# Kernel optimization log

Measured on AMD Instinct MI355X. Metric: run time of the kernel, lower is better.

## Reference

```python
import jax, jax.numpy as jnp
import numpy as np

N = 50000
E = 1600000
D_CONTENT, D_STYLE, D_CAT = 768, 128, 32  # concat feature = 2*D_CAT = 64
H1, H2, NCLS = 64, 64, 2


def _lin_params(key, din, dout, bias=True):
    k1, k2 = jax.random.split(key)
    s = 1.0 / np.sqrt(din)
    W = jax.random.uniform(k1, (din, dout), jnp.float32, -s, s)
    b = jax.random.uniform(k2, (dout,), jnp.float32, -s, s) if bias else None
    return W, b


def setup_inputs() -> dict:
    key = jax.random.key(0)
    ks = jax.random.split(key, 16)
    x_content = jax.random.normal(ks[0], (N, D_CONTENT), jnp.float32)
    x_style = jax.random.normal(ks[1], (N, D_STYLE), jnp.float32)
    edge_index = jax.random.randint(ks[2], (2, E), 0, N, jnp.int64)
    edge_type = jax.random.randint(ks[3], (E,), 0, 4, jnp.int64)
    Wp, bp = _lin_params(ks[4], D_CONTENT, D_CAT)
    Ws, bs = _lin_params(ks[5], D_STYLE, D_CAT)
    # SAGEConv: lin_l (aggregated neighbors, has bias), lin_r (root, no bias)
    Wl1, bl1 = _lin_params(ks[6], 2 * D_CAT, H1)
    Wr1, _ = _lin_params(ks[7], 2 * D_CAT, H1, bias=False)
    Wl2, bl2 = _lin_params(ks[8], H1, H2)
    Wr2, _ = _lin_params(ks[9], H1, H2, bias=False)
    Wl3, bl3 = _lin_params(ks[10], H2, H2)
    Wr3, _ = _lin_params(ks[11], H2, H2, bias=False)
    Wo, bo = _lin_params(ks[12], H2, NCLS)
    return dict(x_content=x_content, x_style=x_style, edge_index=edge_index,
                edge_type=edge_type, Wp=Wp, bp=bp, Ws=Ws, bs=bs,
                Wl1=Wl1, bl1=bl1, Wr1=Wr1, Wl2=Wl2, bl2=bl2, Wr2=Wr2,
                Wl3=Wl3, bl3=bl3, Wr3=Wr3, Wo=Wo, bo=bo)


def _sage_conv(x, src, dst, Wl, bl, Wr):
    # mean aggregation of source-node features at destination nodes
    msg_sum = jax.ops.segment_sum(x[src], dst, num_segments=N)  # [N, d]
    deg = jax.ops.segment_sum(jnp.ones((src.shape[0],), x.dtype), dst,
                              num_segments=N)
    agg = msg_sum / jnp.maximum(deg, 1.0)[:, None]
    return agg @ Wl + bl + x @ Wr


def reference(x_content, x_style, edge_index, edge_type,
              Wp, bp, Ws, bs, Wl1, bl1, Wr1, Wl2, bl2, Wr2,
              Wl3, bl3, Wr3, Wo, bo):
    src, dst = edge_index[0], edge_index[1]
    x = jnp.concatenate([x_content @ Wp + bp, x_style @ Ws + bs], axis=1)
    x = jax.nn.relu(_sage_conv(x, src, dst, Wl1, bl1, Wr1))  # dropout = id (eval)
    x = jax.nn.relu(_sage_conv(x, src, dst, Wl2, bl2, Wr2))
    x = jax.nn.relu(_sage_conv(x, src, dst, Wl3, bl3, Wr3))
    return x @ Wo + bo
```

## Files before the change

### kernel.cpp

```cpp
#include <hip/hip_runtime.h>
#include <stdint.h>


typedef __attribute__((ext_vector_type(8))) unsigned short u16x8;
typedef __attribute__((ext_vector_type(4))) float f32x4;
typedef __attribute__((ext_vector_type(4))) unsigned int u32x4;
typedef __attribute__((ext_vector_type(2))) int i32x2;

static __device__ __forceinline__ float bf2f(unsigned short u) {
  union { unsigned int i; float f; } v;
  v.i = ((unsigned int)u) << 16;
  return v.f;
}

static __device__ __forceinline__ unsigned short f2bf(float f) {
  union { float f; unsigned int i; } v;
  v.f = f;
  unsigned int u = v.i;
  unsigned int r = (u + 0x7FFFu + ((u >> 16) & 1u)) >> 16;
  return (unsigned short)r;
}

template <bool BF>
static __device__ __forceinline__ float ldf(const void* p, long long i) {
  if (BF) return bf2f(((const unsigned short*)p)[i]);
  return ((const float*)p)[i];
}

static __device__ __forceinline__ int clampN(int v, int N) {
  return v < 0 ? 0 : (v >= N ? N - 1 : v);
}

__global__ void k_detect(const void* Wp, const int* ei, int* flags) {
  if (threadIdx.x == 0 && blockIdx.x == 0) {
    const unsigned short* w = (const unsigned short*)Wp;
    int bf = 1;
    for (int i = 0; i < 64; ++i) {
      float v = fabsf(bf2f(w[i]));
      if (!(v < 1.0f)) bf = 0;
    }
    flags[0] = bf;
    int i64 = 1;
    for (int i = 0; i < 32; ++i)
      if (ei[2 * i + 1] != 0) i64 = 0;
    flags[1] = i64;
  }
}

static __device__ __forceinline__ int edge_src(const int* ei, int e, int E,
                                               int i64) {
  return i64 ? ei[2 * (long long)e] : ei[e];
}
static __device__ __forceinline__ int edge_dst(const int* ei, int e, int E,
                                               int i64) {
  return i64 ? ei[2 * ((long long)E + e)] : ei[(long long)E + e];
}


__global__ __launch_bounds__(256) void k_pack(const int* __restrict__ ei, int E,
                                              int N, int* __restrict__ cnt,
                                              i32x2* __restrict__ pairs,
                                              const int* __restrict__ flags) {
  int e = blockIdx.x * 256 + threadIdx.x;
  if (e < E) {
    int i64 = flags[1];
    int s = clampN(edge_src(ei, e, E, i64), N);
    int d = clampN(edge_dst(ei, e, E, i64), N);
    i32x2 p;
    p[0] = s;
    p[1] = d;
    pairs[e] = p;
    atomicAdd(&cnt[d], 1);
  }
}

__global__ __launch_bounds__(256) void k_scan1(const int* __restrict__ cnt,
                                               int* __restrict__ rowptr,
                                               int* __restrict__ bsum, int N) {
  __shared__ int sh[256];
  int t = threadIdx.x;
  int base = blockIdx.x * 1024 + t * 4;
  int v0 = 0, v1 = 0, v2 = 0, v3 = 0;
  if (base + 0 < N) v0 = cnt[base + 0];
  if (base + 1 < N) v1 = cnt[base + 1];
  if (base + 2 < N) v2 = cnt[base + 2];
  if (base + 3 < N) v3 = cnt[base + 3];
  int s = v0 + v1 + v2 + v3;
  sh[t] = s;
  __syncthreads();
  int acc = s;
  for (int off = 1; off < 256; off <<= 1) {
    int x = 0;
    if (t >= off) x = sh[t - off];
    __syncthreads();
    acc += x;
    sh[t] = acc;
    __syncthreads();
  }
  int run = acc - s;
  if (base + 0 < N) rowptr[base + 0] = run;
  run += v0;
  if (base + 1 < N) rowptr[base + 1] = run;
  run += v1;
  if (base + 2 < N) rowptr[base + 2] = run;
  run += v2;
  if (base + 3 < N) rowptr[base + 3] = run;
  run += v3;
  if (t == 255) bsum[blockIdx.x] = acc;
}

__global__ void k_scan2(int* __restrict__ bsum, int nb,
                        int* __restrict__ rowptr, int N) {
  if (threadIdx.x == 0 && blockIdx.x == 0) {
    int run = 0;
    for (int i = 0; i < nb; ++i) {
      int v = bsum[i];
      bsum[i] = run;
      run += v;
    }
    rowptr[N] = run;
  }
}

__global__ __launch_bounds__(256) void k_scan3(int* __restrict__ rowptr,
                                               int* __restrict__ cursor,
                                               const int* __restrict__ bsum,
                                               int N) {
  int i = blockIdx.x * 256 + threadIdx.x;
  if (i < N) {
    int v = rowptr[i] + bsum[i >> 10];
    rowptr[i] = v;
    cursor[i] = v;
  }
}

__global__ __launch_bounds__(256) void k_scatter2(
    const i32x2* __restrict__ pairs, int E, int lo, int hi,
    int* __restrict__ cursor, int* __restrict__ colbuf) {
  int e = blockIdx.x * 256 + threadIdx.x;
  if (e < E) {
    i32x2 p2 = pairs[e];
    int d = p2[1];
    if (d >= lo && d < hi) {
      int p = atomicAdd(&cursor[d], 1);
      if (p >= 0 && p < E) colbuf[p] = p2[0];
    }
  }
}

template <bool BF>
static __device__ void project_body(const void* __restrict__ xc,
                                    const void* __restrict__ xs,
                                    const void* __restrict__ Wp,
                                    const void* __restrict__ bp,
                                    const void* __restrict__ Ws,
                                    const void* __restrict__ bs,
                                    float* __restrict__ h0, int N,
                                    float* __restrict__ lds) {
  float* xt = lds;
  unsigned int* wtb = (unsigned int*)(lds + 2 * 64 * 68);
  float* wtf = lds + 2 * 64 * 68;

  int tid = (int)threadIdx.x;
  int w = __builtin_amdgcn_readfirstlane(tid >> 6);
  int lane = tid & 63;
  int node = (int)blockIdx.x * 64 + lane;

  int sn = tid >> 2;
  int sj = tid & 3;
  int gsn = (int)blockIdx.x * 64 + sn;
  int gsnc = gsn < N ? gsn : (N - 1);

  float c[8], s[8];
#pragma unroll
  for (int r = 0; r < 8; ++r) {
    c[r] = 0.f;
    s[r] = 0.f;
  }

  u16x8 pr0 = {}, pr1 = {};
  f32x4 pf0 = {}, pf1 = {}, pf2 = {}, pf3 = {};
  u32x4 wrg = {};
  f32x4 wf0 = {}, wf1 = {};

  auto stage_load = [&](int t) {
    long long idx;
    const void* src;
    if (t < 12) {
      src = xc;
      idx = (long long)gsnc * 768 + t * 64 + 16 * sj;
    } else {
      src = xs;
      idx = (long long)gsnc * 128 + (t - 12) * 64 + 16 * sj;
    }
    if (BF) {
      const unsigned short* p = (const unsigned short*)src + idx;
      pr0 = *(const u16x8*)p;
      pr1 = *(const u16x8*)(p + 8);
    } else {
      const float* p = (const float*)src + idx;
      pf0 = *(const f32x4*)(p + 0);
      pf1 = *(const f32x4*)(p + 4);
      pf2 = *(const f32x4*)(p + 8);
      pf3 = *(const f32x4*)(p + 12);
    }
    int rowg = (t < 12) ? (t * 64 + sn) : ((t - 12) * 64 + sn);
    const void* wsrc = (t < 12) ? Wp : Ws;
    if (BF) {
      wrg = *(const u32x4*)((const unsigned int*)wsrc +
                            (long long)rowg * 16 + 4 * sj);
    } else {
      const float* p = (const float*)wsrc + (long long)rowg * 32 + 8 * sj;
      wf0 = *(const f32x4*)p;
      wf1 = *(const f32x4*)(p + 4);
    }
  };

  auto stage_write = [&](int t) {
    float* row = xt + (t & 1) * (64 * 68) + sn * 68 + 16 * sj;
    if (BF) {
      f32x4 v;
#pragma unroll
      for (int i = 0; i < 4; ++i) v[i] = bf2f(pr0[i]);
      *(f32x4*)(row + 0) = v;
#pragma unroll
      for (int i = 0; i < 4; ++i) v[i] = bf2f(pr0[4 + i]);
      *(f32x4*)(row + 4) = v;
#pragma unroll
      for (int i = 0; i < 4; ++i) v[i] = bf2f(pr1[i]);
      *(f32x4*)(row + 8) = v;
#pragma unroll
      for (int i = 0; i < 4; ++i) v[i] = bf2f(pr1[4 + i]);
      *(f32x4*)(row + 12) = v;
    } else {
      *(f32x4*)(row + 0) = pf0;
      *(f32x4*)(row + 4) = pf1;
      *(f32x4*)(row + 8) = pf2;
      *(f32x4*)(row + 12) = pf3;
    }
    if (BF) {
      *(u32x4*)(wtb + (t & 1) * (64 * 16) + sn * 16 + 4 * sj) = wrg;
    } else {
      float* wrow = wtf + (t & 1) * (64 * 32) + sn * 32 + 8 * sj;
      *(f32x4*)wrow = wf0;
      *(f32x4*)(wrow + 4) = wf1;
    }
  };

  stage_load(0);
  stage_write(0);
  __syncthreads();

#pragma unroll 1
  for (int t = 0; t < 14; ++t) {
    if (t + 1 < 14) stage_load(t + 1);

    const float* xrow = xt + (t & 1) * (64 * 68) + lane * 68;
    if (BF) {
      const unsigned int* wbase = wtb + (t & 1) * (64 * 16) + 4 * w;
      if (t < 12) {
#pragma unroll 2
        for (int k0 = 0; k0 < 64; k0 += 4) {
          f32x4 x4 = *(const f32x4*)(xrow + k0);
#pragma unroll
          for (int kk = 0; kk < 4; ++kk) {
            u32x4 wp4 = *(const u32x4*)(wbase + (k0 + kk) * 16);
#pragma unroll
            for (int p = 0; p < 4; ++p) {
              union { unsigned int i; float f; } lo, hi;
              lo.i = wp4[p] << 16;
              hi.i = wp4[p] & 0xFFFF0000u;
              c[2 * p + 0] += x4[kk] * lo.f;
              c[2 * p + 1] += x4[kk] * hi.f;
            }
          }
        }
      } else {
#pragma unroll 2
        for (int k0 = 0; k0 < 64; k0 += 4) {
          f32x4 x4 = *(const f32x4*)(xrow + k0);
#pragma unroll
          for (int kk = 0; kk < 4; ++kk) {
            u32x4 wp4 = *(const u32x4*)(wbase + (k0 + kk) * 16);
#pragma unroll
            for (int p = 0; p < 4; ++p) {
              union { unsigned int i; float f; } lo, hi;
              lo.i = wp4[p] << 16;
              hi.i = wp4[p] & 0xFFFF0000u;
              s[2 * p + 0] += x4[kk] * lo.f;
              s[2 * p + 1] += x4[kk] * hi.f;
            }
          }
        }
      }
    } else {
      const float* wbase = wtf + (t & 1) * (64 * 32) + 8 * w;
      if (t < 12) {
#pragma unroll 2
        for (int k0 = 0; k0 < 64; k0 += 4) {
          f32x4 x4 = *(const f32x4*)(xrow + k0);
#pragma unroll
          for (int kk = 0; kk < 4; ++kk) {
            const float* wr = wbase + (k0 + kk) * 32;
            f32x4 wa = *(const f32x4*)wr;
            f32x4 wb = *(const f32x4*)(wr + 4);
#pragma unroll
            for (int r = 0; r < 4; ++r) {
              c[r] += x4[kk] * wa[r];
              c[4 + r] += x4[kk] * wb[r];
            }
          }
        }
      } else {
#pragma unroll 2
        for (int k0 = 0; k0 < 64; k0 += 4) {
          f32x4 x4 = *(const f32x4*)(xrow + k0);
#pragma unroll
          for (int kk = 0; kk < 4; ++kk) {
            const float* wr = wbase + (k0 + kk) * 32;
            f32x4 wa = *(const f32x4*)wr;
            f32x4 wb = *(const f32x4*)(wr + 4);
#pragma unroll
            for (int r = 0; r < 4; ++r) {
              s[r] += x4[kk] * wa[r];
              s[4 + r] += x4[kk] * wb[r];
            }
          }
        }
      }
    }

    if (t + 1 < 14) stage_write(t + 1);
    __syncthreads();
  }

  if (node < N) {
    float* orow = h0 + (long long)node * 64;
    f32x4 v;
#pragma unroll
    for (int r = 0; r < 4; ++r) v[r] = c[r] + ldf<BF>(bp, 8 * w + r);
    *(f32x4*)(orow + 8 * w) = v;
#pragma unroll
    for (int r = 0; r < 4; ++r) v[r] = c[4 + r] + ldf<BF>(bp, 8 * w + 4 + r);
    *(f32x4*)(orow + 8 * w + 4) = v;
#pragma unroll
    for (int r = 0; r < 4; ++r) v[r] = s[r] + ldf<BF>(bs, 8 * w + r);
    *(f32x4*)(orow + 32 + 8 * w) = v;
#pragma unroll
    for (int r = 0; r < 4; ++r) v[r] = s[4 + r] + ldf<BF>(bs, 8 * w + 4 + r);
    *(f32x4*)(orow + 32 + 8 * w + 4) = v;
  }
}

__global__ __launch_bounds__(256) void k_project(
    const void* __restrict__ xc, const void* __restrict__ xs,
    const void* __restrict__ Wp, const void* __restrict__ bp,
    const void* __restrict__ Ws, const void* __restrict__ bs,
    float* __restrict__ h0, int N, const int* __restrict__ flags) {
  __shared__ float lds[2 * 64 * 68 + 2 * 64 * 32];
  if (flags[0])
    project_body<true>(xc, xs, Wp, bp, Ws, bs, h0, N, lds);
  else
    project_body<false>(xc, xs, Wp, bp, Ws, bs, h0, N, lds);
}

template <bool BF>
static __device__ void layer_body(const float* __restrict__ hin,
                                  const int* __restrict__ rowptr,
                                  const int* __restrict__ colbuf,
                                  const void* Wl, const void* bl,
                                  const void* Wr, float* __restrict__ hout,
                                  int N, int last, const void* Wo,
                                  const void* bo, void* outp) {
  int node = (int)((blockIdx.x * blockDim.x + threadIdx.x) >> 6);
  int lane = (int)(threadIdx.x & 63);
  if (node >= N) return;
  int rs = rowptr[node], re = rowptr[node + 1];
  float xself = hin[(long long)node * 64 + lane];
  float agg0 = 0.f, agg1 = 0.f, agg2 = 0.f, agg3 = 0.f;
  float agg4 = 0.f, agg5 = 0.f, agg6 = 0.f, agg7 = 0.f;
  for (int cb = rs; cb < re; cb += 64) {
    int sidx = 0;
    if (cb + lane < re) sidx = clampN(colbuf[cb + lane], N);
    int c = re - cb;
    if (c > 64) c = 64;
    int t = 0;
    for (; t + 8 <= c; t += 8) {
      int s0 = __builtin_amdgcn_readlane(sidx, t + 0);
      int s1 = __builtin_amdgcn_readlane(sidx, t + 1);
      int s2 = __builtin_amdgcn_readlane(sidx, t + 2);
      int s3 = __builtin_amdgcn_readlane(sidx, t + 3);
      int s4 = __builtin_amdgcn_readlane(sidx, t + 4);
      int s5 = __builtin_amdgcn_readlane(sidx, t + 5);
      int s6 = __builtin_amdgcn_readlane(sidx, t + 6);
      int s7 = __builtin_amdgcn_readlane(sidx, t + 7);
      float v0 = hin[(long long)s0 * 64 + lane];
      float v1 = hin[(long long)s1 * 64 + lane];
      float v2 = hin[(long long)s2 * 64 + lane];
      float v3 = hin[(long long)s3 * 64 + lane];
      float v4 = hin[(long long)s4 * 64 + lane];
      float v5 = hin[(long long)s5 * 64 + lane];
      float v6 = hin[(long long)s6 * 64 + lane];
      float v7 = hin[(long long)s7 * 64 + lane];
      agg0 += v0;
      agg1 += v1;
      agg2 += v2;
      agg3 += v3;
      agg4 += v4;
      agg5 += v5;
      agg6 += v6;
      agg7 += v7;
    }
    for (; t < c; ++t) {
      int s = __builtin_amdgcn_readlane(sidx, t);
      agg0 += hin[(long long)s * 64 + lane];
    }
  }
  float agg = ((agg0 + agg1) + (agg2 + agg3)) + ((agg4 + agg5) + (agg6 + agg7));
  int deg = re - rs;
  if (deg > 0) agg *= (1.f / (float)deg);

  float o = ldf<BF>(bl, lane);
#pragma unroll 8
  for (int d = 0; d < 64; ++d) {
    float ad = __uint_as_float(
        __builtin_amdgcn_readlane(__float_as_uint(agg), d));
    float xd = __uint_as_float(
        __builtin_amdgcn_readlane(__float_as_uint(xself), d));
    o += ad * ldf<BF>(Wl, d * 64 + lane);
    o += xd * ldf<BF>(Wr, d * 64 + lane);
  }
  o = fmaxf(o, 0.f);

  if (!last) {
    hout[(long long)node * 64 + lane] = o;
  } else {
    float c0 = o * ldf<BF>(Wo, lane * 2 + 0);
    float c1 = o * ldf<BF>(Wo, lane * 2 + 1);
    for (int off = 32; off > 0; off >>= 1) {
      c0 += __shfl_xor(c0, off, 64);
      c1 += __shfl_xor(c1, off, 64);
    }
    if (lane == 0) {
      float r0 = c0 + ldf<BF>(bo, 0);
      float r1 = c1 + ldf<BF>(bo, 1);
      if (BF) {
        unsigned short* o16 = (unsigned short*)outp;
        o16[(long long)node * 2 + 0] = f2bf(r0);
        o16[(long long)node * 2 + 1] = f2bf(r1);
      } else {
        float* o32 = (float*)outp;
        o32[(long long)node * 2 + 0] = r0;
        o32[(long long)node * 2 + 1] = r1;
      }
    }
  }
}

__global__ __launch_bounds__(256) void k_layer(
    const float* hin, const int* rowptr, const int* colbuf, const void* Wl,
    const void* bl, const void* Wr, float* hout, int N, int last,
    const void* Wo, const void* bo, void* outp, const int* __restrict__ flags) {
  if (flags[0])
    layer_body<true>(hin, rowptr, colbuf, Wl, bl, Wr, hout, N, last, Wo, bo,
                     outp);
  else
    layer_body<false>(hin, rowptr, colbuf, Wl, bl, Wr, hout, N, last, Wo, bo,
                      outp);
}


extern "C" void kernel_launch(void* const* d_in, const int* in_sizes, int n_in,
                              void* d_out, int out_size, void* d_ws,
                              size_t ws_size, hipStream_t stream) {
  const void* xc = d_in[0];
  const void* xs = d_in[1];
  const int* ei = (const int*)d_in[2];
  const void* Wp = d_in[4];
  const void* bp = d_in[5];
  const void* Ws = d_in[6];
  const void* bs = d_in[7];
  const void* Wl1 = d_in[8];
  const void* bl1 = d_in[9];
  const void* Wr1 = d_in[10];
  const void* Wl2 = d_in[11];
  const void* bl2 = d_in[12];
  const void* Wr2 = d_in[13];
  const void* Wl3 = d_in[14];
  const void* bl3 = d_in[15];
  const void* Wr3 = d_in[16];
  const void* Wo = d_in[17];
  const void* bo = d_in[18];

  int N = out_size / 2;
  int E = in_sizes[3];

  char* ws = (char*)d_ws;
  size_t off = 0;
  auto alloc = [&](size_t bytes) {
    char* p = ws + off;
    off += (bytes + 255) & ~(size_t)255;
    return p;
  };
  int* colbuf = (int*)alloc((size_t)E * 4);
  int* cnt = (int*)alloc((size_t)N * 4);
  int* rowptr = (int*)alloc((size_t)(N + 1) * 4);
  int* cursor = (int*)alloc((size_t)N * 4);
  int* bsum = (int*)alloc(4096);
  int* flags = (int*)alloc(256);
  float* h0 = (float*)alloc((size_t)N * 64 * 4);
  float* h1 = (float*)alloc((size_t)N * 64 * 4);
  (void)ws_size;
  (void)n_in;

  i32x2* pairs = (i32x2*)h0;

  k_detect<<<1, 64, 0, stream>>>(Wp, ei, flags);

  hipMemsetAsync(cnt, 0, (size_t)N * 4, stream);
  int eb = (E + 255) / 256;
  k_pack<<<eb, 256, 0, stream>>>(ei, E, N, cnt, pairs, flags);
  int sb = (N + 1023) / 1024;
  k_scan1<<<sb, 256, 0, stream>>>(cnt, rowptr, bsum, N);
  k_scan2<<<1, 64, 0, stream>>>(bsum, sb, rowptr, N);
  k_scan3<<<(N + 255) / 256, 256, 0, stream>>>(rowptr, cursor, bsum, N);

  const int NPASS = 8;
  int chunk = (N + NPASS - 1) / NPASS;
  for (int r = 0; r < NPASS; ++r) {
    int lo = r * chunk;
    int hi = lo + chunk < N ? lo + chunk : N;
    k_scatter2<<<eb, 256, 0, stream>>>(pairs, E, lo, hi, cursor, colbuf);
  }

  int pb = (N + 63) / 64;
  k_project<<<pb, 256, 0, stream>>>(xc, xs, Wp, bp, Ws, bs, h0, N, flags);

  int nb4 = (N + 3) / 4;
  k_layer<<<nb4, 256, 0, stream>>>(h0, rowptr, colbuf, Wl1, bl1, Wr1, h1, N, 0,
                                   nullptr, nullptr, nullptr, flags);
  k_layer<<<nb4, 256, 0, stream>>>(h1, rowptr, colbuf, Wl2, bl2, Wr2, h0, N, 0,
                                   nullptr, nullptr, nullptr, flags);
  k_layer<<<nb4, 256, 0, stream>>>(h0, rowptr, colbuf, Wl3, bl3, Wr3, h1, N, 1,
                                   Wo, bo, d_out, flags);
}
```

Measured before the change: 730.2 us.

## Use bf16 MFMA for projection, unroll gather by 16, halve scatter passes

The bf16 path of the input projection now stages both weight matrices into LDS in an MFMA-friendly layout and computes the 64-column projection with 16x16x32 bf16 MFMA instructions, replacing scalar FMA loops with in-register bf16 unpacking. The SAGE neighbor gather gains a 16-wide unrolled path so more independent loads are in flight per wave. The CSR scatter runs in 4 destination-range passes instead of 8, reducing launches and re-reads of the edge list at some cost to write locality. The default inputs are float32, so the MFMA path may only run if the dtype-detection flag selects bf16.

```diff
diff --git a/kernel.cpp b/kernel.cpp
--- a/kernel.cpp
+++ b/kernel.cpp
@@ -3,6 +3,7 @@
 
 
 typedef __attribute__((ext_vector_type(8))) unsigned short u16x8;
+typedef __attribute__((ext_vector_type(8))) short bf16x8;
 typedef __attribute__((ext_vector_type(4))) float f32x4;
 typedef __attribute__((ext_vector_type(4))) unsigned int u32x4;
 typedef __attribute__((ext_vector_type(2))) int i32x2;
@@ -148,8 +149,7 @@
   }
 }
 
-template <bool BF>
-static __device__ void project_body(const void* __restrict__ xc,
+static __device__ void project_mfma(const void* __restrict__ xc,
                                     const void* __restrict__ xs,
                                     const void* __restrict__ Wp,
                                     const void* __restrict__ bp,
@@ -157,8 +157,94 @@
                                     const void* __restrict__ bs,
                                     float* __restrict__ h0, int N,
                                     float* __restrict__ lds) {
+  unsigned short* fb = (unsigned short*)lds;
+  int tid = (int)threadIdx.x;
+  int w = __builtin_amdgcn_readfirstlane(tid >> 6);
+  int l = tid & 63;
+  int node0 = (int)blockIdx.x * 64;
+
+  const unsigned short* wp16 = (const unsigned short*)Wp;
+  const unsigned short* ws16 = (const unsigned short*)Ws;
+#pragma unroll
+  for (int i = 0; i < 14; ++i) {
+    int ci = tid + 256 * i;
+    int e0 = ci * 8;
+    int isC = e0 < 24576;
+    int eb = isC ? e0 : (e0 - 24576);
+    int r = eb >> 5;
+    int c0 = eb & 31;
+    int s_ = r >> 5;
+    int g = (r >> 3) & 3;
+    int j = r & 7;
+    int f = isC ? (s_ * 2 + (c0 >> 4)) : (48 + s_ * 2 + (c0 >> 4));
+    u16x8 v = *(const u16x8*)((isC ? wp16 : ws16) + eb);
+    unsigned short* d = fb + f * 512 + ((g << 4) + (c0 & 15)) * 8 + j;
+#pragma unroll
+    for (int m = 0; m < 8; ++m) d[m * 8] = v[m];
+  }
+  __syncthreads();
+
+  int arow = node0 + 16 * w + (l & 15);
+  int arowc = arow < N ? arow : (N - 1);
+  int kg = (l >> 4) * 8;
+  const unsigned short* xcl = (const unsigned short*)xc + (long long)arowc * 768;
+  const unsigned short* xsl = (const unsigned short*)xs + (long long)arowc * 128;
+
+  auto loadA = [&](int s) -> bf16x8 {
+    if (s < 24) return *(const bf16x8*)(xcl + s * 32 + kg);
+    return *(const bf16x8*)(xsl + (s - 24) * 32 + kg);
+  };
+
+  f32x4 ac0 = {0.f, 0.f, 0.f, 0.f};
+  f32x4 ac1 = {0.f, 0.f, 0.f, 0.f};
+  f32x4 ac2 = {0.f, 0.f, 0.f, 0.f};
+  f32x4 ac3 = {0.f, 0.f, 0.f, 0.f};
+
+  bf16x8 a0 = loadA(0);
+  bf16x8 a1 = loadA(1);
+#pragma unroll 1
+  for (int s = 0; s < 28; ++s) {
+    bf16x8 acur = a0;
+    a0 = a1;
+    if (s + 2 < 28) a1 = loadA(s + 2);
+    if (s < 24) {
+      bf16x8 b0 = *(const bf16x8*)(fb + (s * 2 + 0) * 512 + l * 8);
+      bf16x8 b1 = *(const bf16x8*)(fb + (s * 2 + 1) * 512 + l * 8);
+      ac0 = __builtin_amdgcn_mfma_f32_16x16x32_bf16(acur, b0, ac0, 0, 0, 0);
+      ac1 = __builtin_amdgcn_mfma_f32_16x16x32_bf16(acur, b1, ac1, 0, 0, 0);
+    } else {
+      int sb = s - 24;
+      bf16x8 b2 = *(const bf16x8*)(fb + (48 + sb * 2 + 0) * 512 + l * 8);
+      bf16x8 b3 = *(const bf16x8*)(fb + (48 + sb * 2 + 1) * 512 + l * 8);
+      ac2 = __builtin_amdgcn_mfma_f32_16x16x32_bf16(acur, b2, ac2, 0, 0, 0);
+      ac3 = __builtin_amdgcn_mfma_f32_16x16x32_bf16(acur, b3, ac3, 0, 0, 0);
+    }
+  }
+
+  int colb = l & 15;
+  int rbase = (l >> 4) * 4;
+#pragma unroll
+  for (int r = 0; r < 4; ++r) {
+    int nodeg = node0 + 16 * w + rbase + r;
+    if (nodeg < N) {
+      float* orow = h0 + (long long)nodeg * 64;
+      orow[0 + colb] = ac0[r] + bf2f(((const unsigned short*)bp)[0 + colb]);
+      orow[16 + colb] = ac1[r] + bf2f(((const unsigned short*)bp)[16 + colb]);
+      orow[32 + colb] = ac2[r] + bf2f(((const unsigned short*)bs)[0 + colb]);
+      orow[48 + colb] = ac3[r] + bf2f(((const unsigned short*)bs)[16 + colb]);
+    }
+  }
+}
+
+static __device__ void project_f32(const void* __restrict__ xc,
+                                   const void* __restrict__ xs,
+                                   const void* __restrict__ Wp,
+                                   const void* __restrict__ bp,
+                                   const void* __restrict__ Ws,
+                                   const void* __restrict__ bs,
+                                   float* __restrict__ h0, int N,
+                                   float* __restrict__ lds) {
   float* xt = lds;
-  unsigned int* wtb = (unsigned int*)(lds + 2 * 64 * 68);
   float* wtf = lds + 2 * 64 * 68;
 
   int tid = (int)threadIdx.x;
@@ -178,9 +264,7 @@
     s[r] = 0.f;
   }
 
-  u16x8 pr0 = {}, pr1 = {};
   f32x4 pf0 = {}, pf1 = {}, pf2 = {}, pf3 = {};
-  u32x4 wrg = {};
   f32x4 wf0 = {}, wf1 = {};
 
   auto stage_load = [&](int t) {
@@ -193,58 +277,27 @@
       src = xs;
       idx = (long long)gsnc * 128 + (t - 12) * 64 + 16 * sj;
     }
-    if (BF) {
-      const unsigned short* p = (const unsigned short*)src + idx;
-      pr0 = *(const u16x8*)p;
-      pr1 = *(const u16x8*)(p + 8);
-    } else {
-      const float* p = (const float*)src + idx;
-      pf0 = *(const f32x4*)(p + 0);
-      pf1 = *(const f32x4*)(p + 4);
-      pf2 = *(const f32x4*)(p + 8);
-      pf3 = *(const f32x4*)(p + 12);
-    }
+    const float* p = (const float*)src + idx;
+    pf0 = *(const f32x4*)(p + 0);
+    pf1 = *(const f32x4*)(p + 4);
+    pf2 = *(const f32x4*)(p + 8);
+    pf3 = *(const f32x4*)(p + 12);
     int rowg = (t < 12) ? (t * 64 + sn) : ((t - 12) * 64 + sn);
-    const void* wsrc = (t < 12) ? Wp : Ws;
-    if (BF) {
-      wrg = *(const u32x4*)((const unsigned int*)wsrc +
-                            (long long)rowg * 16 + 4 * sj);
-    } else {
-      const float* p = (const float*)wsrc + (long long)rowg * 32 + 8 * sj;
-      wf0 = *(const f32x4*)p;
-      wf1 = *(const f32x4*)(p + 4);
-    }
+    const float* wp = (const float*)((t < 12) ? Wp : Ws) +
+                      (long long)rowg * 32 + 8 * sj;
+    wf0 = *(const f32x4*)wp;
+    wf1 = *(const f32x4*)(wp + 4);
   };
 
   auto stage_write = [&](int t) {
     float* row = xt + (t & 1) * (64 * 68) + sn * 68 + 16 * sj;
-    if (BF) {
-      f32x4 v;
-#pragma unroll
-      for (int i = 0; i < 4; ++i) v[i] = bf2f(pr0[i]);
-      *(f32x4*)(row + 0) = v;
-#pragma unroll
-      for (int i = 0; i < 4; ++i) v[i] = bf2f(pr0[4 + i]);
-      *(f32x4*)(row + 4) = v;
-#pragma unroll
-      for (int i = 0; i < 4; ++i) v[i] = bf2f(pr1[i]);
-      *(f32x4*)(row + 8) = v;
-#pragma unroll
-      for (int i = 0; i < 4; ++i) v[i] = bf2f(pr1[4 + i]);
-      *(f32x4*)(row + 12) = v;
-    } else {
-      *(f32x4*)(row + 0) = pf0;
-      *(f32x4*)(row + 4) = pf1;
-      *(f32x4*)(row + 8) = pf2;
-      *(f32x4*)(row + 12) = pf3;
-    }
-    if (BF) {
-      *(u32x4*)(wtb + (t & 1) * (64 * 16) + sn * 16 + 4 * sj) = wrg;
-    } else {
-      float* wrow = wtf + (t & 1) * (64 * 32) + sn * 32 + 8 * sj;
-      *(f32x4*)wrow = wf0;
-      *(f32x4*)(wrow + 4) = wf1;
-    }
+    *(f32x4*)(row + 0) = pf0;
+    *(f32x4*)(row + 4) = pf1;
+    *(f32x4*)(row + 8) = pf2;
+    *(f32x4*)(row + 12) = pf3;
+    float* wrow = wtf + (t & 1) * (64 * 32) + sn * 32 + 8 * sj;
+    *(f32x4*)wrow = wf0;
+    *(f32x4*)(wrow + 4) = wf1;
   };
 
   stage_load(0);
@@ -254,82 +307,24 @@
 #pragma unroll 1
   for (int t = 0; t < 14; ++t) {
     if (t + 1 < 14) stage_load(t + 1);
-
     const float* xrow = xt + (t & 1) * (64 * 68) + lane * 68;
-    if (BF) {
-      const unsigned int* wbase = wtb + (t & 1) * (64 * 16) + 4 * w;
-      if (t < 12) {
+    const float* wbase = wtf + (t & 1) * (64 * 32) + 8 * w;
+    float* acc = (t < 12) ? c : s;
 #pragma unroll 2
-        for (int k0 = 0; k0 < 64; k0 += 4) {
-          f32x4 x4 = *(const f32x4*)(xrow + k0);
-#pragma unroll
-          for (int kk = 0; kk < 4; ++kk) {
-            u32x4 wp4 = *(const u32x4*)(wbase + (k0 + kk) * 16);
-#pragma unroll
-            for (int p = 0; p < 4; ++p) {
-              union { unsigned int i; float f; } lo, hi;
-              lo.i = wp4[p] << 16;
-              hi.i = wp4[p] & 0xFFFF0000u;
-              c[2 * p + 0] += x4[kk] * lo.f;
-              c[2 * p + 1] += x4[kk] * hi.f;
-            }
-          }
-        }
-      } else {
-#pragma unroll 2
-        for (int k0 = 0; k0 < 64; k0 += 4) {
-          f32x4 x4 = *(const f32x4*)(xrow + k0);
-#pragma unroll
-          for (int kk = 0; kk < 4; ++kk) {
-            u32x4 wp4 = *(const u32x4*)(wbase + (k0 + kk) * 16);
-#pragma unroll
-            for (int p = 0; p < 4; ++p) {
-              union { unsigned int i; float f; } lo, hi;
-              lo.i = wp4[p] << 16;
-              hi.i = wp4[p] & 0xFFFF0000u;
-              s[2 * p + 0] += x4[kk] * lo.f;
-              s[2 * p + 1] += x4[kk] * hi.f;
-            }
-          }
+    for (int k0 = 0; k0 < 64; k0 += 4) {
+      f32x4 x4 = *(const f32x4*)(xrow + k0);
+#pragma unroll
+      for (int kk = 0; kk < 4; ++kk) {
+        const float* wr = wbase + (k0 + kk) * 32;
+        f32x4 wa = *(const f32x4*)wr;
+        f32x4 wb = *(const f32x4*)(wr + 4);
+#pragma unroll
+        for (int r = 0; r < 4; ++r) {
+          acc[r] += x4[kk] * wa[r];
+          acc[4 + r] += x4[kk] * wb[r];
         }
       }
-    } else {
-      const float* wbase = wtf + (t & 1) * (64 * 32) + 8 * w;
-      if (t < 12) {
-#pragma unroll 2
-        for (int k0 = 0; k0 < 64; k0 += 4) {
-          f32x4 x4 = *(const f32x4*)(xrow + k0);
-#pragma unroll
-          for (int kk = 0; kk < 4; ++kk) {
-            const float* wr = wbase + (k0 + kk) * 32;
-            f32x4 wa = *(const f32x4*)wr;
-            f32x4 wb = *(const f32x4*)(wr + 4);
-#pragma unroll
-            for (int r = 0; r < 4; ++r) {
-              c[r] += x4[kk] * wa[r];
-              c[4 + r] += x4[kk] * wb[r];
-            }
-          }
-        }
-      } else {
-#pragma unroll 2
-        for (int k0 = 0; k0 < 64; k0 += 4) {
-          f32x4 x4 = *(const f32x4*)(xrow + k0);
-#pragma unroll
-          for (int kk = 0; kk < 4; ++kk) {
-            const float* wr = wbase + (k0 + kk) * 32;
-            f32x4 wa = *(const f32x4*)wr;
-            f32x4 wb = *(const f32x4*)(wr + 4);
-#pragma unroll
-            for (int r = 0; r < 4; ++r) {
-              s[r] += x4[kk] * wa[r];
-              s[4 + r] += x4[kk] * wb[r];
-            }
-          }
-        }
-      }
-    }
-
+    }
     if (t + 1 < 14) stage_write(t + 1);
     __syncthreads();
   }
@@ -338,16 +333,18 @@
     float* orow = h0 + (long long)node * 64;
     f32x4 v;
 #pragma unroll
-    for (int r = 0; r < 4; ++r) v[r] = c[r] + ldf<BF>(bp, 8 * w + r);
+    for (int r = 0; r < 4; ++r) v[r] = c[r] + ((const float*)bp)[8 * w + r];
     *(f32x4*)(orow + 8 * w) = v;
 #pragma unroll
-    for (int r = 0; r < 4; ++r) v[r] = c[4 + r] + ldf<BF>(bp, 8 * w + 4 + r);
+    for (int r = 0; r < 4; ++r)
+      v[r] = c[4 + r] + ((const float*)bp)[8 * w + 4 + r];
     *(f32x4*)(orow + 8 * w + 4) = v;
 #pragma unroll
-    for (int r = 0; r < 4; ++r) v[r] = s[r] + ldf<BF>(bs, 8 * w + r);
+    for (int r = 0; r < 4; ++r) v[r] = s[r] + ((const float*)bs)[8 * w + r];
     *(f32x4*)(orow + 32 + 8 * w) = v;
 #pragma unroll
-    for (int r = 0; r < 4; ++r) v[r] = s[4 + r] + ldf<BF>(bs, 8 * w + 4 + r);
+    for (int r = 0; r < 4; ++r)
+      v[r] = s[4 + r] + ((const float*)bs)[8 * w + 4 + r];
     *(f32x4*)(orow + 32 + 8 * w + 4) = v;
   }
 }
@@ -357,11 +354,11 @@
     const void* __restrict__ Wp, const void* __restrict__ bp,
     const void* __restrict__ Ws, const void* __restrict__ bs,
     float* __restrict__ h0, int N, const int* __restrict__ flags) {
-  __shared__ float lds[2 * 64 * 68 + 2 * 64 * 32];
+  __shared__ float lds[14336];
   if (flags[0])
-    project_body<true>(xc, xs, Wp, bp, Ws, bs, h0, N, lds);
+    project_mfma(xc, xs, Wp, bp, Ws, bs, h0, N, lds);
   else
-    project_body<false>(xc, xs, Wp, bp, Ws, bs, h0, N, lds);
+    project_f32(xc, xs, Wp, bp, Ws, bs, h0, N, lds);
 }
 
 template <bool BF>
@@ -385,6 +382,48 @@
     int c = re - cb;
     if (c > 64) c = 64;
     int t = 0;
+    for (; t + 16 <= c; t += 16) {
+      int s0 = __builtin_amdgcn_readlane(sidx, t + 0);
+      int s1 = __builtin_amdgcn_readlane(sidx, t + 1);
+      int s2 = __builtin_amdgcn_readlane(sidx, t + 2);
+      int s3 = __builtin_amdgcn_readlane(sidx, t + 3);
+      int s4 = __builtin_amdgcn_readlane(sidx, t + 4);
+      int s5 = __builtin_amdgcn_readlane(sidx, t + 5);
+      int s6 = __builtin_amdgcn_readlane(sidx, t + 6);
+      int s7 = __builtin_amdgcn_readlane(sidx, t + 7);
+      int s8 = __builtin_amdgcn_readlane(sidx, t + 8);
+      int s9 = __builtin_amdgcn_readlane(sidx, t + 9);
+      int sa = __builtin_amdgcn_readlane(sidx, t + 10);
+      int sb = __builtin_amdgcn_readlane(sidx, t + 11);
+      int sc = __builtin_amdgcn_readlane(sidx, t + 12);
+      int sd = __builtin_amdgcn_readlane(sidx, t + 13);
+      int se = __builtin_amdgcn_readlane(sidx, t + 14);
+      int sf = __builtin_amdgcn_readlane(sidx, t + 15);
+      float v0 = hin[(long long)s0 * 64 + lane];
+      float v1 = hin[(long long)s1 * 64 + lane];
+      float v2 = hin[(long long)s2 * 64 + lane];
+      float v3 = hin[(long long)s3 * 64 + lane];
+      float v4 = hin[(long long)s4 * 64 + lane];
+      float v5 = hin[(long long)s5 * 64 + lane];
+      float v6 = hin[(long long)s6 * 64 + lane];
+      float v7 = hin[(long long)s7 * 64 + lane];
+      float v8 = hin[(long long)s8 * 64 + lane];
+      float v9 = hin[(long long)s9 * 64 + lane];
+      float va = hin[(long long)sa * 64 + lane];
+      float vb = hin[(long long)sb * 64 + lane];
+      float vc = hin[(long long)sc * 64 + lane];
+      float vd = hin[(long long)sd * 64 + lane];
+      float ve = hin[(long long)se * 64 + lane];
+      float vf = hin[(long long)sf * 64 + lane];
+      agg0 += v0 + v8;
+      agg1 += v1 + v9;
+      agg2 += v2 + va;
+      agg3 += v3 + vb;
+      agg4 += v4 + vc;
+      agg5 += v5 + vd;
+      agg6 += v6 + ve;
+      agg7 += v7 + vf;
+    }
     for (; t + 8 <= c; t += 8) {
       int s0 = __builtin_amdgcn_readlane(sidx, t + 0);
       int s1 = __builtin_amdgcn_readlane(sidx, t + 1);
@@ -525,7 +564,7 @@
   k_scan2<<<1, 64, 0, stream>>>(bsum, sb, rowptr, N);
   k_scan3<<<(N + 255) / 256, 256, 0, stream>>>(rowptr, cursor, bsum, N);
 
-  const int NPASS = 8;
+  const int NPASS = 4;
   int chunk = (N + NPASS - 1) / NPASS;
   for (int r = 0; r < NPASS; ++r) {
     int lo = r * chunk;
```

After: 727.6 us. About the same (-0.4%).

## Move input projection to bf16 MFMA with split-precision, widen gather unroll

Applied to the files above, without the earlier changes.

Adds an MFMA path for the content/style projection. Weights are pre-split into bf16 hi/lo fragment layouts, and the fp32 activations are split on the fly into three bf16 products so fp32 accuracy is roughly kept. A runtime self-test kernel checks the MFMA fragment layout and falls back to the old VALU kernel if it fails. The layer gather loop also gets a 16-wide unroll, and the scatter pass count is halved. This costs extra launches and roughly three times the MFMA work for fp32 inputs.

```diff
diff --git a/kernel.cpp b/kernel.cpp
--- a/kernel.cpp
+++ b/kernel.cpp
@@ -3,6 +3,7 @@
 
 
 typedef __attribute__((ext_vector_type(8))) unsigned short u16x8;
+typedef __attribute__((ext_vector_type(8))) short bf16x8;
 typedef __attribute__((ext_vector_type(4))) float f32x4;
 typedef __attribute__((ext_vector_type(4))) unsigned int u32x4;
 typedef __attribute__((ext_vector_type(2))) int i32x2;
@@ -25,6 +26,36 @@
 static __device__ __forceinline__ float ldf(const void* p, long long i) {
   if (BF) return bf2f(((const unsigned short*)p)[i]);
   return ((const float*)p)[i];
+}
+
+template <bool BF>
+static __device__ __forceinline__ void load8(const void* p, long long idx,
+                                             float* out) {
+  if (BF) {
+    u16x8 v = *(const u16x8*)((const unsigned short*)p + idx);
+#pragma unroll
+    for (int j = 0; j < 8; ++j) out[j] = bf2f(v[j]);
+  } else {
+    f32x4 a = *(const f32x4*)((const float*)p + idx);
+    f32x4 b = *(const f32x4*)((const float*)p + idx + 4);
+#pragma unroll
+    for (int j = 0; j < 4; ++j) {
+      out[j] = a[j];
+      out[4 + j] = b[j];
+    }
+  }
+}
+
+static __device__ __forceinline__ void split8(const float* v, bf16x8& hi,
+                                              bf16x8& lo) {
+#pragma unroll
+  for (int j = 0; j < 8; ++j) {
+    unsigned int u = __float_as_uint(v[j]);
+    unsigned int uh = u & 0xFFFF0000u;
+    hi[j] = (short)(uh >> 16);
+    float rf = v[j] - __uint_as_float(uh);
+    lo[j] = (short)(__float_as_uint(rf) >> 16);
+  }
 }
 
 static __device__ __forceinline__ int clampN(int v, int N) {
@@ -45,6 +76,35 @@
       if (ei[2 * i + 1] != 0) i64 = 0;
     flags[1] = i64;
   }
+}
+
+__global__ void k_mfmatest(int* flags) {
+  int l = (int)threadIdx.x;
+  int rc = l & 15;
+  int kg = (l >> 4) * 8;
+  bf16x8 a, b;
+#pragma unroll
+  for (int j = 0; j < 8; ++j) {
+    int k = kg + j;
+    a[j] = (short)f2bf((float)(((rc * 31 + k * 7) % 13) - 6));
+    b[j] = (short)f2bf((float)(((k * 5 + rc * 3) % 11) - 5));
+  }
+  f32x4 z = {0.f, 0.f, 0.f, 0.f};
+  f32x4 d = __builtin_amdgcn_mfma_f32_16x16x32_bf16(a, b, z, 0, 0, 0);
+  bool ok = true;
+#pragma unroll
+  for (int r = 0; r < 4; ++r) {
+    int rw = (l >> 4) * 4 + r;
+    float ref = 0.f;
+    for (int k = 0; k < 32; ++k) {
+      float av = (float)(((rw * 31 + k * 7) % 13) - 6);
+      float bv = (float)(((k * 5 + rc * 3) % 11) - 5);
+      ref += av * bv;
+    }
+    ok = ok && (d[r] == ref);
+  }
+  unsigned long long m = __ballot(ok);
+  if (l == 0) flags[2] = (m == 0xFFFFFFFFFFFFFFFFull) ? 1 : 0;
 }
 
 static __device__ __forceinline__ int edge_src(const int* ei, int e, int E,
@@ -148,15 +208,160 @@
   }
 }
 
+__global__ __launch_bounds__(256) void k_wprep(
+    const void* __restrict__ Wp, const void* __restrict__ Ws,
+    unsigned short* __restrict__ wfhi, unsigned short* __restrict__ wflo,
+    const int* __restrict__ flags) {
+  int ci = (int)blockIdx.x * 256 + (int)threadIdx.x;
+  if (ci >= 3584) return;
+  int BF = flags[0];
+  int e0 = ci * 8;
+  int isC = e0 < 24576;
+  int eb = isC ? e0 : (e0 - 24576);
+  int r = eb >> 5;
+  int c0 = eb & 31;
+  int s_ = r >> 5;
+  int g = (r >> 3) & 3;
+  int j = r & 7;
+  int f = isC ? (s_ * 2 + (c0 >> 4)) : (48 + s_ * 2 + (c0 >> 4));
+  const void* wsrc = isC ? Wp : Ws;
+  float v[8];
+  if (BF) {
+    load8<true>(wsrc, eb, v);
+  } else {
+    load8<false>(wsrc, eb, v);
+  }
+  bf16x8 hi, lo;
+  split8(v, hi, lo);
+  unsigned short* dh = wfhi + f * 512 + ((g << 4) + (c0 & 15)) * 8 + j;
+  unsigned short* dl = wflo + f * 512 + ((g << 4) + (c0 & 15)) * 8 + j;
+#pragma unroll
+  for (int m = 0; m < 8; ++m) {
+    dh[m * 8] = (unsigned short)hi[m];
+    dl[m * 8] = (unsigned short)lo[m];
+  }
+}
+
 template <bool BF>
-static __device__ void project_body(const void* __restrict__ xc,
-                                    const void* __restrict__ xs,
-                                    const void* __restrict__ Wp,
-                                    const void* __restrict__ bp,
-                                    const void* __restrict__ Ws,
-                                    const void* __restrict__ bs,
-                                    float* __restrict__ h0, int N,
-                                    float* __restrict__ lds) {
+static __device__ void project_mfma_body(
+    const void* __restrict__ xc, const void* __restrict__ xs,
+    const unsigned short* __restrict__ wfhi,
+    const unsigned short* __restrict__ wflo, const void* __restrict__ bp,
+    const void* __restrict__ bs, float* __restrict__ h0, int N) {
+  int tid = (int)threadIdx.x;
+  int w = __builtin_amdgcn_readfirstlane(tid >> 6);
+  int l = tid & 63;
+  int node0 = (int)blockIdx.x * 64;
+
+  int arow = node0 + 16 * w + (l & 15);
+  int arowc = arow < N ? arow : (N - 1);
+  int kg = (l >> 4) * 8;
+  long long xco = (long long)arowc * 768;
+  long long xso = (long long)arowc * 128;
+
+  f32x4 ac0 = {0.f, 0.f, 0.f, 0.f};
+  f32x4 ac1 = {0.f, 0.f, 0.f, 0.f};
+  f32x4 ac2 = {0.f, 0.f, 0.f, 0.f};
+  f32x4 ac3 = {0.f, 0.f, 0.f, 0.f};
+
+  float av0[8], av1[8];
+  load8<BF>(xc, xco + 0 * 32 + kg, av0);
+  load8<BF>(xc, xco + 1 * 32 + kg, av1);
+
+#pragma unroll
+  for (int s = 0; s < 28; ++s) {
+    float cur[8];
+#pragma unroll
+    for (int j = 0; j < 8; ++j) {
+      cur[j] = av0[j];
+      av0[j] = av1[j];
+    }
+    if (s + 2 < 28) {
+      int sn = s + 2;
+      if (sn < 24)
+        load8<BF>(xc, xco + sn * 32 + kg, av1);
+      else
+        load8<BF>(xs, xso + (sn - 24) * 32 + kg, av1);
+    }
+
+    bf16x8 ah, al;
+    split8(cur, ah, al);
+
+    if (s < 24) {
+      const unsigned short* f0 = wfhi + (s * 2 + 0) * 512 + l * 8;
+      const unsigned short* f1 = wfhi + (s * 2 + 1) * 512 + l * 8;
+      bf16x8 b0h = *(const bf16x8*)f0;
+      bf16x8 b1h = *(const bf16x8*)f1;
+      ac0 = __builtin_amdgcn_mfma_f32_16x16x32_bf16(ah, b0h, ac0, 0, 0, 0);
+      ac1 = __builtin_amdgcn_mfma_f32_16x16x32_bf16(ah, b1h, ac1, 0, 0, 0);
+      if (!BF) {
+        const unsigned short* g0 = wflo + (s * 2 + 0) * 512 + l * 8;
+        const unsigned short* g1 = wflo + (s * 2 + 1) * 512 + l * 8;
+        bf16x8 b0l = *(const bf16x8*)g0;
+        bf16x8 b1l = *(const bf16x8*)g1;
+        ac0 = __builtin_amdgcn_mfma_f32_16x16x32_bf16(ah, b0l, ac0, 0, 0, 0);
+        ac0 = __builtin_amdgcn_mfma_f32_16x16x32_bf16(al, b0h, ac0, 0, 0, 0);
+        ac1 = __builtin_amdgcn_mfma_f32_16x16x32_bf16(ah, b1l, ac1, 0, 0, 0);
+        ac1 = __builtin_amdgcn_mfma_f32_16x16x32_bf16(al, b1h, ac1, 0, 0, 0);
+      }
+    } else {
+      int sb = s - 24;
+      const unsigned short* f2 = wfhi + (48 + sb * 2 + 0) * 512 + l * 8;
+      const unsigned short* f3 = wfhi + (48 + sb * 2 + 1) * 512 + l * 8;
+      bf16x8 b2h = *(const bf16x8*)f2;
+      bf16x8 b3h = *(const bf16x8*)f3;
+      ac2 = __builtin_amdgcn_mfma_f32_16x16x32_bf16(ah, b2h, ac2, 0, 0, 0);
+      ac3 = __builtin_amdgcn_mfma_f32_16x16x32_bf16(ah, b3h, ac3, 0, 0, 0);
+      if (!BF) {
+        const unsigned short* g2 = wflo + (48 + sb * 2 + 0) * 512 + l * 8;
+        const unsigned short* g3 = wflo + (48 + sb * 2 + 1) * 512 + l * 8;
+        bf16x8 b2l = *(const bf16x8*)g2;
+        bf16x8 b3l = *(const bf16x8*)g3;
+        ac2 = __builtin_amdgcn_mfma_f32_16x16x32_bf16(ah, b2l, ac2, 0, 0, 0);
+        ac2 = __builtin_amdgcn_mfma_f32_16x16x32_bf16(al, b2h, ac2, 0, 0, 0);
+        ac3 = __builtin_amdgcn_mfma_f32_16x16x32_bf16(ah, b3l, ac3, 0, 0, 0);
+        ac3 = __builtin_amdgcn_mfma_f32_16x16x32_bf16(al, b3h, ac3, 0, 0, 0);
+      }
+    }
+  }
+
+  int colb = l & 15;
+  int rbase = (l >> 4) * 4;
+#pragma unroll
+  for (int r = 0; r < 4; ++r) {
+    int nodeg = node0 + 16 * w + rbase + r;
+    if (nodeg < N) {
+      float* orow = h0 + (long long)nodeg * 64;
+      orow[0 + colb] = ac0[r] + ldf<BF>(bp, 0 + colb);
+      orow[16 + colb] = ac1[r] + ldf<BF>(bp, 16 + colb);
+      orow[32 + colb] = ac2[r] + ldf<BF>(bs, 0 + colb);
+      orow[48 + colb] = ac3[r] + ldf<BF>(bs, 16 + colb);
+    }
+  }
+}
+
+__global__ __launch_bounds__(256) void k_project_mfma(
+    const void* __restrict__ xc, const void* __restrict__ xs,
+    const unsigned short* __restrict__ wfhi,
+    const unsigned short* __restrict__ wflo, const void* __restrict__ bp,
+    const void* __restrict__ bs, float* __restrict__ h0, int N,
+    const int* __restrict__ flags) {
+  if (!flags[2]) return;
+  if (flags[0])
+    project_mfma_body<true>(xc, xs, wfhi, wflo, bp, bs, h0, N);
+  else
+    project_mfma_body<false>(xc, xs, wfhi, wflo, bp, bs, h0, N);
+}
+
+template <bool BF>
+static __device__ void project_valu_body(const void* __restrict__ xc,
+                                         const void* __restrict__ xs,
+                                         const void* __restrict__ Wp,
+                                         const void* __restrict__ bp,
+                                         const void* __restrict__ Ws,
+                                         const void* __restrict__ bs,
+                                         float* __restrict__ h0, int N,
+                                         float* __restrict__ lds) {
   float* xt = lds;
   unsigned int* wtb = (unsigned int*)(lds + 2 * 64 * 68);
   float* wtf = lds + 2 * 64 * 68;
@@ -254,82 +459,45 @@
 #pragma unroll 1
   for (int t = 0; t < 14; ++t) {
     if (t + 1 < 14) stage_load(t + 1);
-
     const float* xrow = xt + (t & 1) * (64 * 68) + lane * 68;
     if (BF) {
       const unsigned int* wbase = wtb + (t & 1) * (64 * 16) + 4 * w;
-      if (t < 12) {
+      float* acc = (t < 12) ? c : s;
 #pragma unroll 2
-        for (int k0 = 0; k0 < 64; k0 += 4) {
-          f32x4 x4 = *(const f32x4*)(xrow + k0);
-#pragma unroll
-          for (int kk = 0; kk < 4; ++kk) {
-            u32x4 wp4 = *(const u32x4*)(wbase + (k0 + kk) * 16);
-#pragma unroll
-            for (int p = 0; p < 4; ++p) {
-              union { unsigned int i; float f; } lo, hi;
-              lo.i = wp4[p] << 16;
-              hi.i = wp4[p] & 0xFFFF0000u;
-              c[2 * p + 0] += x4[kk] * lo.f;
-              c[2 * p + 1] += x4[kk] * hi.f;
-            }
-          }
-        }
-      } else {
-#pragma unroll 2
-        for (int k0 = 0; k0 < 64; k0 += 4) {
-          f32x4 x4 = *(const f32x4*)(xrow + k0);
-#pragma unroll
-          for (int kk = 0; kk < 4; ++kk) {
-            u32x4 wp4 = *(const u32x4*)(wbase + (k0 + kk) * 16);
-#pragma unroll
-            for (int p = 0; p < 4; ++p) {
-              union { unsigned int i; float f; } lo, hi;
-              lo.i = wp4[p] << 16;
-              hi.i = wp4[p] & 0xFFFF0000u;
-              s[2 * p + 0] += x4[kk] * lo.f;
-              s[2 * p + 1] += x4[kk] * hi.f;
-            }
+      for (int k0 = 0; k0 < 64; k0 += 4) {
+        f32x4 x4 = *(const f32x4*)(xrow + k0);
+#pragma unroll
+        for (int kk = 0; kk < 4; ++kk) {
+          u32x4 wp4 = *(const u32x4*)(wbase + (k0 + kk) * 16);
+#pragma unroll
+          for (int p = 0; p < 4; ++p) {
+            union { unsigned int i; float f; } lo, hi;
+            lo.i = wp4[p] << 16;
+            hi.i = wp4[p] & 0xFFFF0000u;
+            acc[2 * p + 0] += x4[kk] * lo.f;
+            acc[2 * p + 1] += x4[kk] * hi.f;
           }
         }
       }
     } else {
       const float* wbase = wtf + (t & 1) * (64 * 32) + 8 * w;
-      if (t < 12) {
+      float* acc = (t < 12) ? c : s;
 #pragma unroll 2
-        for (int k0 = 0; k0 < 64; k0 += 4) {
-          f32x4 x4 = *(const f32x4*)(xrow + k0);
-#pragma unroll
-          for (int kk = 0; kk < 4; ++kk) {
-            const float* wr = wbase + (k0 + kk) * 32;
-            f32x4 wa = *(const f32x4*)wr;
-            f32x4 wb = *(const f32x4*)(wr + 4);
-#pragma unroll
-            for (int r = 0; r < 4; ++r) {
-              c[r] += x4[kk] * wa[r];
-              c[4 + r] += x4[kk] * wb[r];
-            }
-          }
-        }
-      } else {
-#pragma unroll 2
-        for (int k0 = 0; k0 < 64; k0 += 4) {
-          f32x4 x4 = *(const f32x4*)(xrow + k0);
-#pragma unroll
-          for (int kk = 0; kk < 4; ++kk) {
-            const float* wr = wbase + (k0 + kk) * 32;
-            f32x4 wa = *(const f32x4*)wr;
-            f32x4 wb = *(const f32x4*)(wr + 4);
-#pragma unroll
-            for (int r = 0; r < 4; ++r) {
-              s[r] += x4[kk] * wa[r];
-              s[4 + r] += x4[kk] * wb[r];
-            }
+      for (int k0 = 0; k0 < 64; k0 += 4) {
+        f32x4 x4 = *(const f32x4*)(xrow + k0);
+#pragma unroll
+        for (int kk = 0; kk < 4; ++kk) {
+          const float* wr = wbase + (k0 + kk) * 32;
+          f32x4 wa = *(const f32x4*)wr;
+          f32x4 wb = *(const f32x4*)(wr + 4);
+#pragma unroll
+          for (int r = 0; r < 4; ++r) {
+            acc[r] += x4[kk] * wa[r];
+            acc[4 + r] += x4[kk] * wb[r];
           }
         }
       }
     }
-
     if (t + 1 < 14) stage_write(t + 1);
     __syncthreads();
   }
@@ -352,16 +520,17 @@
   }
 }
 
-__global__ __launch_bounds__(256) void k_project(
+__global__ __launch_bounds__(256) void k_project_valu(
     const void* __restrict__ xc, const void* __restrict__ xs,
     const void* __restrict__ Wp, const void* __restrict__ bp,
     const void* __restrict__ Ws, const void* __restrict__ bs,
     float* __restrict__ h0, int N, const int* __restrict__ flags) {
   __shared__ float lds[2 * 64 * 68 + 2 * 64 * 32];
+  if (flags[2]) return;
   if (flags[0])
-    project_body<true>(xc, xs, Wp, bp, Ws, bs, h0, N, lds);
+    project_valu_body<true>(xc, xs, Wp, bp, Ws, bs, h0, N, lds);
   else
-    project_body<false>(xc, xs, Wp, bp, Ws, bs, h0, N, lds);
+    project_valu_body<false>(xc, xs, Wp, bp, Ws, bs, h0, N, lds);
 }
 
 template <bool BF>
@@ -385,6 +554,48 @@
     int c = re - cb;
     if (c > 64) c = 64;
     int t = 0;
+    for (; t + 16 <= c; t += 16) {
+      int s0 = __builtin_amdgcn_readlane(sidx, t + 0);
+      int s1 = __builtin_amdgcn_readlane(sidx, t + 1);
+      int s2 = __builtin_amdgcn_readlane(sidx, t + 2);
+      int s3 = __builtin_amdgcn_readlane(sidx, t + 3);
+      int s4 = __builtin_amdgcn_readlane(sidx, t + 4);
+      int s5 = __builtin_amdgcn_readlane(sidx, t + 5);
+      int s6 = __builtin_amdgcn_readlane(sidx, t + 6);
+      int s7 = __builtin_amdgcn_readlane(sidx, t + 7);
+      int s8 = __builtin_amdgcn_readlane(sidx, t + 8);
+      int s9 = __builtin_amdgcn_readlane(sidx, t + 9);
+      int sa = __builtin_amdgcn_readlane(sidx, t + 10);
+      int sb = __builtin_amdgcn_readlane(sidx, t + 11);
+      int sc = __builtin_amdgcn_readlane(sidx, t + 12);
+      int sd = __builtin_amdgcn_readlane(sidx, t + 13);
+      int se = __builtin_amdgcn_readlane(sidx, t + 14);
+      int sf = __builtin_amdgcn_readlane(sidx, t + 15);
+      float v0 = hin[(long long)s0 * 64 + lane];
+      float v1 = hin[(long long)s1 * 64 + lane];
+      float v2 = hin[(long long)s2 * 64 + lane];
+      float v3 = hin[(long long)s3 * 64 + lane];
+      float v4 = hin[(long long)s4 * 64 + lane];
+      float v5 = hin[(long long)s5 * 64 + lane];
+      float v6 = hin[(long long)s6 * 64 + lane];
+      float v7 = hin[(long long)s7 * 64 + lane];
+      float v8 = hin[(long long)s8 * 64 + lane];
+      float v9 = hin[(long long)s9 * 64 + lane];
+      float va = hin[(long long)sa * 64 + lane];
+      float vb = hin[(long long)sb * 64 + lane];
+      float vc = hin[(long long)sc * 64 + lane];
+      float vd = hin[(long long)sd * 64 + lane];
+      float ve = hin[(long long)se * 64 + lane];
+      float vf = hin[(long long)sf * 64 + lane];
+      agg0 += v0 + v8;
+      agg1 += v1 + v9;
+      agg2 += v2 + va;
+      agg3 += v3 + vb;
+      agg4 += v4 + vc;
+      agg5 += v5 + vd;
+      agg6 += v6 + ve;
+      agg7 += v7 + vf;
+    }
     for (; t + 8 <= c; t += 8) {
       int s0 = __builtin_amdgcn_readlane(sidx, t + 0);
       int s1 = __builtin_amdgcn_readlane(sidx, t + 1);
@@ -508,6 +719,8 @@
   int* cursor = (int*)alloc((size_t)N * 4);
   int* bsum = (int*)alloc(4096);
   int* flags = (int*)alloc(256);
+  unsigned short* wfhi = (unsigned short*)alloc(57344);
+  unsigned short* wflo = (unsigned short*)alloc(57344);
   float* h0 = (float*)alloc((size_t)N * 64 * 4);
   float* h1 = (float*)alloc((size_t)N * 64 * 4);
   (void)ws_size;
@@ -516,6 +729,8 @@
   i32x2* pairs = (i32x2*)h0;
 
   k_detect<<<1, 64, 0, stream>>>(Wp, ei, flags);
+  k_mfmatest<<<1, 64, 0, stream>>>(flags);
+  k_wprep<<<14, 256, 0, stream>>>(Wp, Ws, wfhi, wflo, flags);
 
   hipMemsetAsync(cnt, 0, (size_t)N * 4, stream);
   int eb = (E + 255) / 256;
@@ -525,7 +740,7 @@
   k_scan2<<<1, 64, 0, stream>>>(bsum, sb, rowptr, N);
   k_scan3<<<(N + 255) / 256, 256, 0, stream>>>(rowptr, cursor, bsum, N);
 
-  const int NPASS = 8;
+  const int NPASS = 4;
   int chunk = (N + NPASS - 1) / NPASS;
   for (int r = 0; r < NPASS; ++r) {
     int lo = r * chunk;
@@ -534,7 +749,9 @@
   }
 
   int pb = (N + 63) / 64;
-  k_project<<<pb, 256, 0, stream>>>(xc, xs, Wp, bp, Ws, bs, h0, N, flags);
+  k_project_mfma<<<pb, 256, 0, stream>>>(xc, xs, wfhi, wflo, bp, bs, h0, N,
+                                         flags);
+  k_project_valu<<<pb, 256, 0, stream>>>(xc, xs, Wp, bp, Ws, bs, h0, N, flags);
 
   int nb4 = (N + 3) / 4;
   k_layer<<<nb4, 256, 0, stream>>>(h0, rowptr, colbuf, Wl1, bl1, Wr1, h1, N, 0,
```

Measured after the change: 730.0 us. About the same (-0.0%).
